# Kernel optimization log

Hardware: AMD Instinct MI355X
Metric: run time of the kernel (lower is better)

Reference implementation:

```python
import itertools
import jax, jax.numpy as jnp
import numpy as np

ORDER = 3  # MaskDE(order=3) -> DescartesExtension orders 2..3
D = 80
B = 8192


def setup_inputs() -> dict:
    key = jax.random.key(0)
    kx, km = jax.random.split(key)
    x = jax.random.normal(kx, (B, D), dtype=jnp.float32)
    mask = jax.random.randint(km, (D,), 0, 2).astype(jnp.bool_)
    return {"x": x, "mask": mask}


def _comb_indices(m: int, order: int) -> np.ndarray:
    # combinations with replacement of range(m), shape (n_comb, order)
    return np.array(list(itertools.combinations_with_replacement(range(m), order)), dtype=np.int32)


def reference(x, mask):
    # mask is a concrete bool vector: masked_select == static gather
    idx = np.flatnonzero(np.asarray(mask))  # (m,)
    m = idx.size
    xm = x[:, idx]  # (B, m)
    parts = [xm]
    for order in range(2, ORDER + 1):
        combs = _comb_indices(m, order)           # (C, order)
        # gather-multiply-reduce: prod of each feature combination
        parts.append(jnp.prod(xm[:, combs], axis=-1))  # (B, C)
    return jnp.concatenate(parts, axis=-1)
```

## Files before the change

kernel.cpp:

```cpp
#include <hip/hip_runtime.h>
#include <stdint.h>

#define DMAX   80
#define BLK    256
#define XW     96
#define XL     64
#define EPBMAX 16384
#define NR     3

typedef float f32x4 __attribute__((ext_vector_type(4)));

__global__ void maskde_setup(const void* __restrict__ mask_raw, int m,
                             int* __restrict__ idx_out,
                             uint16_t* __restrict__ pair16,
                             uint16_t* __restrict__ tab16,
                             uint32_t* __restrict__ tab32,
                             int use16, int tpad, int T, int P) {
    int tid = blockIdx.x * blockDim.x + threadIdx.x;

    if (tid == 0) {
        const uint8_t* b8  = (const uint8_t*)mask_raw;
        const int*     b32 = (const int*)mask_raw;
        const float*   bf  = (const float*)mask_raw;
        int cnt = 0; bool ok = true;
        for (int i = 0; i < DMAX; ++i) { uint8_t v = b8[i]; if (v > 1) ok = false; cnt += (v != 0); }
        int mode;
        if (ok && cnt == m) {
            mode = 0;
        } else {
            cnt = 0; ok = true;
            for (int i = 0; i < DMAX; ++i) { int v = b32[i]; if (v != 0 && v != 1) ok = false; cnt += (v != 0); }
            mode = (ok && cnt == m) ? 1 : 2;
        }
        int k = 0;
        for (int i = 0; i < DMAX && k < m; ++i) {
            bool on = (mode == 0) ? (b8[i] != 0)
                    : (mode == 1) ? (b32[i] != 0)
                                  : (bf[i] != 0.0f);
            if (on) idx_out[k++] = i;
        }
    }

    int stride = gridDim.x * blockDim.x;
    for (int p = tid; p < P; p += stride) {
        int rem = p, i = 0;
        while (rem >= m - i) { rem -= (m - i); ++i; }
        int j = i + rem;

        pair16[p] = (uint16_t)(i | (j << 8));

        #define WR4(c, pf, kf) do {                                          \
            int _c = (c);                                                    \
            if (use16) {                                                     \
                uint16_t _v = (uint16_t)((pf) | ((kf) << 10));               \
                tab16[_c] = _v;                                              \
                if (_c >= 1) tab16[tpad     + _c - 1] = _v;                  \
                if (_c >= 2) tab16[2 * tpad + _c - 2] = _v;                  \
                if (_c >= 3) tab16[3 * tpad + _c - 3] = _v;                  \
            } else {                                                         \
                uint32_t _v = (uint32_t)(pf) | ((uint32_t)(kf) << 16);       \
                tab32[_c] = _v;                                              \
                if (_c >= 1) tab32[tpad     + _c - 1] = _v;                  \
                if (_c >= 2) tab32[2 * tpad + _c - 2] = _v;                  \
                if (_c >= 3) tab32[3 * tpad + _c - 3] = _v;                  \
            }                                                                \
        } while (0)

        if (p < m) WR4(p, P, p);
        WR4(m + p, p, m);

        int mi = m - i;
        long long Si  = ((long long)m * (m + 1) * (m + 2)
                       - (long long)mi * (mi + 1) * (mi + 2)) / 6;
        int Rij = ((m - i) + (m - j + 1)) * (j - i) / 2;
        int base = m + P + (int)Si + Rij;
        for (int k3 = j; k3 < m; ++k3)
            WR4(base + (k3 - j), p, k3);
        #undef WR4
    }
}

__global__ void maskde_xsel(const float* __restrict__ x,
                            const int* __restrict__ idx,
                            float* __restrict__ xsel, int m, int rows) {
    int g = blockIdx.x * BLK + threadIdx.x;
    int total = rows * XW;
    for (; g < total; g += gridDim.x * BLK) {
        int row = g / XW, k = g - row * XW;
        xsel[g] = (k < m) ? x[row * DMAX + idx[k]] : 1.0f;
    }
}

template<bool U16>
__global__ __launch_bounds__(BLK) void
maskde_expand(const float* __restrict__ xsel,
              const uint16_t* __restrict__ pair16,
              const uint16_t* __restrict__ tab16,
              const uint32_t* __restrict__ tab32,
              int tpad, float* __restrict__ out,
              int m, int T, int P, int rows, int epb, int total) {
    extern __shared__ float sm[];
    const int PPS = P + 1;
    float* xls = sm;
    float* pps = sm + NR * XL;

    const int tid  = threadIdx.x;
    const int e0   = blockIdx.x * epb;
    const int eend = min(e0 + epb, total);
    const int r0   = e0 / T;

    for (int q = tid; q < NR * XL; q += BLK) {
        int rr = q >> 6, k = q & (XL - 1);
        int row = r0 + rr;
        xls[q] = (row < rows) ? xsel[row * XW + k] : 1.0f;
    }
    __syncthreads();

    for (int rr = 0; rr < NR; ++rr) {
        int row = r0 + rr;
        if (row >= rows) break;
        const float* xr = xls + rr * XL;
        float*       pr = pps + rr * PPS;
        for (int p = tid; p <= P; p += BLK) {
            float v = 1.0f;
            if (p < P) {
                uint32_t ij = pair16[p];
                v = xr[ij & 0xFF] * xr[(ij >> 8) & 0xFF];
            }
            pr[p] = v;
        }
    }
    __syncthreads();

    int a = e0;
    for (int rr = 0; rr < NR && a < eend; ++rr) {
        const int row = r0 + rr;
        const long long rowend = (long long)(row + 1) * T;
        const int b = (int)(rowend < (long long)eend ? rowend : (long long)eend);
        const float* xr = xls + rr * XL;
        const float* pr = pps + rr * PPS;
        const int cbase = a - row * T;

        int ahead = a + ((4 - (a & 3)) & 3);
        if (ahead > b) ahead = b;

        if (tid < ahead - a) {
            int c = cbase + tid;
            uint32_t p_, k_;
            if constexpr (U16) { uint16_t t = tab16[c]; p_ = t & 0x3FF; k_ = t >> 10; }
            else               { uint32_t t = tab32[c]; p_ = t & 0xFFFF; k_ = t >> 16; }
            out[a + tid] = pr[p_] * xr[k_];
        }

        const int nq    = (b - ahead) >> 2;
        const int calig = cbase + (ahead - a);
        const int s4    = calig & 3;

        if constexpr (U16) {
            const uint16_t* tb = tab16 + (size_t)s4 * tpad + (calig - s4);
            for (int q = tid; q < nq; q += BLK) {
                uint2 t = *(const uint2*)(tb + 4 * q);
                f32x4 o;
                o.x = pr[t.x & 0x3FF]         * xr[(t.x >> 10) & 0x3F];
                o.y = pr[(t.x >> 16) & 0x3FF] * xr[t.x >> 26];
                o.z = pr[t.y & 0x3FF]         * xr[(t.y >> 10) & 0x3F];
                o.w = pr[(t.y >> 16) & 0x3FF] * xr[t.y >> 26];
                *(f32x4*)(out + ahead + 4 * q) = o;
            }
        } else {
            const uint32_t* tb = tab32 + (size_t)s4 * tpad + (calig - s4);
            for (int q = tid; q < nq; q += BLK) {
                uint4 t = *(const uint4*)(tb + 4 * q);
                f32x4 o;
                o.x = pr[t.x & 0xFFFF] * xr[t.x >> 16];
                o.y = pr[t.y & 0xFFFF] * xr[t.y >> 16];
                o.z = pr[t.z & 0xFFFF] * xr[t.z >> 16];
                o.w = pr[t.w & 0xFFFF] * xr[t.w >> 16];
                *(f32x4*)(out + ahead + 4 * q) = o;
            }
        }

        const int ts = ahead + 4 * nq;
        if (tid < b - ts) {
            int c = cbase + (ts - a) + tid;
            uint32_t p_, k_;
            if constexpr (U16) { uint16_t t = tab16[c]; p_ = t & 0x3FF; k_ = t >> 10; }
            else               { uint32_t t = tab32[c]; p_ = t & 0xFFFF; k_ = t >> 16; }
            out[ts + tid] = pr[p_] * xr[k_];
        }
        a = b;
    }
}

extern "C" void kernel_launch(void* const* d_in, const int* in_sizes, int n_in,
                              void* d_out, int out_size, void* d_ws, size_t ws_size,
                              hipStream_t stream) {
    const float* x    = (const float*)d_in[0];
    const void*  mask = d_in[1];
    float*       out  = (float*)d_out;

    int rows = in_sizes[0] / DMAX;
    if (rows <= 0 || out_size <= 0) return;
    long long Tll = (long long)out_size / rows;

    int m = -1;
    for (int mm = 0; mm <= DMAX; ++mm) {
        long long t = (long long)mm
                    + (long long)mm * (mm + 1) / 2
                    + (long long)mm * (mm + 1) * (mm + 2) / 6;
        if (t == Tll) { m = mm; break; }
    }
    if (m <= 0) return;

    int T     = (int)Tll;
    int P     = m * (m + 1) / 2;
    int tpad  = (T + 3) & ~3;
    int total = rows * T;
    int use16 = (P < 1024 && m < 63) ? 1 : 0;

    int epb = EPBMAX;
    if (epb > 2 * T) epb = T & ~3;
    if (epb < 4) epb = 4;

    char* ws = (char*)d_ws;
    int*      idx    = (int*)ws;
    uint16_t* pair16 = (uint16_t*)(ws + 1024);
    uint16_t* tab16  = (uint16_t*)(ws + 32768);
    uint32_t* tab32  = (uint32_t*)(ws + 32768);
    size_t off_xsel  = 32768 + (size_t)4 * tpad * 4 + 256;
    off_xsel = (off_xsel + 255) & ~(size_t)255;
    float*    xsel   = (float*)(ws + off_xsel);

    int sblocks = (P + 255) / 256;
    if (sblocks < 1) sblocks = 1;
    maskde_setup<<<sblocks, 256, 0, stream>>>(mask, m, idx, pair16, tab16,
                                              tab32, use16, tpad, T, P);

    int xblocks = (rows * XW + BLK - 1) / BLK;
    if (xblocks > 2048) xblocks = 2048;
    maskde_xsel<<<xblocks, BLK, 0, stream>>>(x, idx, xsel, m, rows);

    int nb = (total + epb - 1) / epb;
    size_t shmem = (size_t)(NR * XL + NR * (P + 1)) * sizeof(float);
    if (use16)
        maskde_expand<true><<<nb, BLK, shmem, stream>>>(xsel, pair16, tab16,
                                                        tab32, tpad, out, m, T,
                                                        P, rows, epb, total);
    else
        maskde_expand<false><<<nb, BLK, shmem, stream>>>(xsel, pair16, tab16,
                                                         tab32, tpad, out, m, T,
                                                         P, rows, epb, total);
}
```

Baseline: 140.6 us.

## Precompute pairwise products in a separate kernel and shrink expand blocks

Adds a kernel that computes all pairwise products per row into a global workspace buffer. The expand kernel then loads them into shared memory with vectorized copies instead of recomputing them per block. Elements per block drop from 16384 to 2048 and rows per block from 3 to 2, giving many more, smaller blocks for better load balance and occupancy. In exchange it adds an extra launch and a global write/read of the pairwise table per row.

After: 193.4 us. +37.5%, slower.

```diff
diff --git a/kernel.cpp b/kernel.cpp
--- a/kernel.cpp
+++ b/kernel.cpp
@@ -4,9 +4,8 @@
 #define DMAX   80
 #define BLK    256
 #define XW     96
-#define XL     64
-#define EPBMAX 16384
-#define NR     3
+#define EPBMAX 2048
+#define NR     2
 
 typedef float f32x4 __attribute__((ext_vector_type(4)));
 
@@ -91,44 +90,52 @@
     }
 }
 
+__global__ void maskde_ppsall(const float* __restrict__ xsel,
+                              const uint16_t* __restrict__ pair16,
+                              float* __restrict__ ppsall, int P, int PPW) {
+    int p   = blockIdx.x * BLK + threadIdx.x;
+    int row = blockIdx.y;
+    if (p >= PPW) return;
+    float v = 1.0f;
+    if (p < P) {
+        uint32_t ij = pair16[p];
+        const float* xr = xsel + row * XW;
+        v = xr[ij & 0xFF] * xr[(ij >> 8) & 0xFF];
+    }
+    ppsall[(size_t)row * PPW + p] = v;
+}
+
 template<bool U16>
 __global__ __launch_bounds__(BLK) void
 maskde_expand(const float* __restrict__ xsel,
-              const uint16_t* __restrict__ pair16,
+              const float* __restrict__ ppsall,
               const uint16_t* __restrict__ tab16,
               const uint32_t* __restrict__ tab32,
               int tpad, float* __restrict__ out,
-              int m, int T, int P, int rows, int epb, int total) {
+              int T, int PPW, int rows, int epb, int total) {
+    constexpr int XLT = U16 ? 64 : XW;
     extern __shared__ float sm[];
-    const int PPS = P + 1;
     float* xls = sm;
-    float* pps = sm + NR * XL;
-
-    const int tid  = threadIdx.x;
-    const int e0   = blockIdx.x * epb;
-    const int eend = min(e0 + epb, total);
-    const int r0   = e0 / T;
-
-    for (int q = tid; q < NR * XL; q += BLK) {
-        int rr = q >> 6, k = q & (XL - 1);
+    float* pps = sm + NR * XLT;
+
+    const int tid = threadIdx.x;
+    const int e0  = blockIdx.x * epb;
+    if (e0 >= total) return;
+    const int eend = (e0 + epb < total) ? e0 + epb : total;
+    const int r0 = e0 / T;
+
+    for (int q = tid; q < NR * XLT; q += BLK) {
+        int rr = q / XLT, k = q - rr * XLT;
         int row = r0 + rr;
         xls[q] = (row < rows) ? xsel[row * XW + k] : 1.0f;
     }
-    __syncthreads();
-
-    for (int rr = 0; rr < NR; ++rr) {
+    const int nu4 = PPW >> 2;
+    for (int q = tid; q < NR * nu4; q += BLK) {
+        int rr = q / nu4, u = q - rr * nu4;
         int row = r0 + rr;
-        if (row >= rows) break;
-        const float* xr = xls + rr * XL;
-        float*       pr = pps + rr * PPS;
-        for (int p = tid; p <= P; p += BLK) {
-            float v = 1.0f;
-            if (p < P) {
-                uint32_t ij = pair16[p];
-                v = xr[ij & 0xFF] * xr[(ij >> 8) & 0xFF];
-            }
-            pr[p] = v;
-        }
+        if (row < rows)
+            *(f32x4*)(pps + rr * PPW + 4 * u) =
+                *(const f32x4*)(ppsall + (size_t)row * PPW + 4 * u);
     }
     __syncthreads();
 
@@ -137,8 +144,8 @@
         const int row = r0 + rr;
         const long long rowend = (long long)(row + 1) * T;
         const int b = (int)(rowend < (long long)eend ? rowend : (long long)eend);
-        const float* xr = xls + rr * XL;
-        const float* pr = pps + rr * PPS;
+        const float* xr = xls + rr * XLT;
+        const float* pr = pps + rr * PPW;
         const int cbase = a - row * T;
 
         int ahead = a + ((4 - (a & 3)) & 3);
@@ -214,12 +221,13 @@
 
     int T     = (int)Tll;
     int P     = m * (m + 1) / 2;
+    int PPW   = (P + 1 + 3) & ~3;
     int tpad  = (T + 3) & ~3;
     int total = rows * T;
     int use16 = (P < 1024 && m < 63) ? 1 : 0;
 
     int epb = EPBMAX;
-    if (epb > 2 * T) epb = T & ~3;
+    if (epb > T) epb = T & ~3;
     if (epb < 4) epb = 4;
 
     char* ws = (char*)d_ws;
@@ -230,6 +238,9 @@
     size_t off_xsel  = 32768 + (size_t)4 * tpad * 4 + 256;
     off_xsel = (off_xsel + 255) & ~(size_t)255;
     float*    xsel   = (float*)(ws + off_xsel);
+    size_t off_pps   = off_xsel + (size_t)rows * XW * 4;
+    off_pps = (off_pps + 255) & ~(size_t)255;
+    float*    ppsall = (float*)(ws + off_pps);
 
     int sblocks = (P + 255) / 256;
     if (sblocks < 1) sblocks = 1;
@@ -240,14 +251,17 @@
     if (xblocks > 2048) xblocks = 2048;
     maskde_xsel<<<xblocks, BLK, 0, stream>>>(x, idx, xsel, m, rows);
 
+    dim3 pgrid((PPW + BLK - 1) / BLK, rows);
+    maskde_ppsall<<<pgrid, BLK, 0, stream>>>(xsel, pair16, ppsall, P, PPW);
+
     int nb = (total + epb - 1) / epb;
-    size_t shmem = (size_t)(NR * XL + NR * (P + 1)) * sizeof(float);
+    size_t shmem = (size_t)(NR * XW + NR * PPW) * sizeof(float);
     if (use16)
-        maskde_expand<true><<<nb, BLK, shmem, stream>>>(xsel, pair16, tab16,
-                                                        tab32, tpad, out, m, T,
-                                                        P, rows, epb, total);
+        maskde_expand<true><<<nb, BLK, shmem, stream>>>(xsel, ppsall, tab16,
+                                                        tab32, tpad, out, T,
+                                                        PPW, rows, epb, total);
     else
-        maskde_expand<false><<<nb, BLK, shmem, stream>>>(xsel, pair16, tab16,
-                                                         tab32, tpad, out, m, T,
-                                                         P, rows, epb, total);
-}
+        maskde_expand<false><<<nb, BLK, shmem, stream>>>(xsel, ppsall, tab16,
+                                                         tab32, tpad, out, T,
+                                                         PPW, rows, epb, total);
+}
```
